# Performance work log

Hardware: AMD Instinct MI355X
Metric: run time of the kernel (lower is better)

Reference implementation:

```python
import jax, jax.numpy as jnp
import numpy as np

BOX_WARP = 1.2
BMIN, BMAX = -0.6, 0.6   # sampler bbox
EPS_FD = 0.01            # finite-difference eps for SDF normals
RADIUS = 0.5             # sphere sdf bias radius
INV_S = 80.0             # sdf -> density sharpness (softplus clamp mode)
S_PER_RAY = 96


def _grid_sample_one(feat, uv):
    # feat: [C,H,W]; uv: [M,2] in [-1,1]; bilinear, align_corners=False, zeros padding
    C, H, W = feat.shape
    x = ((uv[:, 0] + 1.0) * W - 1.0) * 0.5
    y = ((uv[:, 1] + 1.0) * H - 1.0) * 0.5
    x0 = jnp.floor(x).astype(jnp.int32)
    y0 = jnp.floor(y).astype(jnp.int32)
    wx = x - x0
    wy = y - y0

    def g(ix, iy):
        valid = ((ix >= 0) & (ix < W) & (iy >= 0) & (iy < H)).astype(feat.dtype)
        v = feat[:, jnp.clip(iy, 0, H - 1), jnp.clip(ix, 0, W - 1)]  # [C,M]
        return v * valid[None, :]

    out = (g(x0, y0) * (1 - wx) * (1 - wy) + g(x0 + 1, y0) * wx * (1 - wy)
           + g(x0, y0 + 1) * (1 - wx) * wy + g(x0 + 1, y0 + 1) * wx * wy)
    return out.T  # [M,C]


def sample_from_planes(planes, coords):
    # planes: [N,3,C,H,W]; coords: [N,M,3] -> [N,M,3*C]
    N, P, C, H, W = planes.shape
    M = coords.shape[1]
    nc = coords * (2.0 / BOX_WARP)
    proj = jnp.stack([nc[..., (0, 1)], nc[..., (0, 2)], nc[..., (1, 2)]], axis=1)  # [N,3,M,2]
    s = jax.vmap(_grid_sample_one)(planes.reshape(N * P, C, H, W), proj.reshape(N * P, M, 2))
    return s.reshape(N, P, M, C).transpose(0, 2, 1, 3).reshape(N, M, P * C)


def decode(planes, coords, W1, b1, W2, b2):
    x = sample_from_planes(planes, coords)
    return jax.nn.relu(x @ W1 + b1) @ W2 + b2  # [N,M,4]


def render(planes, ro, rd, W1, b1, W2, b2):
    N, R, _ = ro.shape
    S = S_PER_RAY
    safe_rd = jnp.where(jnp.abs(rd) < 1e-9, 1e-9, rd)
    t1 = (BMIN - ro) / safe_rd
    t2 = (BMAX - ro) / safe_rd
    tn = jnp.maximum(jnp.max(jnp.minimum(t1, t2), axis=-1), 0.0)   # [N,R] ray_start (auto box)
    tf = jnp.min(jnp.maximum(t1, t2), axis=-1)                      # [N,R] ray_end
    span = jnp.maximum(tf - tn, 0.0)
    frac = (jnp.arange(S, dtype=ro.dtype) + 0.5) / S
    depths = tn[..., None] + span[..., None] * frac                 # [N,R,S]
    pts = (ro[:, :, None, :] + depths[..., None] * rd[:, :, None, :]).reshape(N, R * S, 3)

    x = decode(planes, pts, W1, b1, W2, b2)
    sdf = x[..., 0:1]
    rgb = jax.nn.sigmoid(x[..., 1:]) * (1 + 2 * 0.001) - 0.001

    # finite-difference SDF gradient (3 extra decoder passes)
    eye = jnp.eye(3, dtype=pts.dtype) * EPS_FD
    sdf_off = jnp.stack(
        [decode(planes, jnp.clip(pts + eye[i], BMIN, BMAX), W1, b1, W2, b2)[..., 0] for i in range(3)],
        axis=-1)                                                    # [N,M,3]
    sdf_grad = (sdf_off - sdf) / EPS_FD
    normal = sdf_grad / (jnp.linalg.norm(sdf_grad, axis=-1, keepdims=True) + 1e-8)

    # sphere sdf bias, sdf -> density, alpha compositing
    shifted = sdf[..., 0] + (jnp.linalg.norm(pts, axis=-1) - RADIUS)
    sigma = jax.nn.softplus(-shifted * INV_S).reshape(N, R, S)
    delta = (span / S)[..., None]
    alpha = 1.0 - jnp.exp(-sigma * delta)
    T = jnp.cumprod(1.0 - alpha + 1e-10, axis=-1)
    T = jnp.concatenate([jnp.ones_like(T[..., :1]), T[..., :-1]], axis=-1)
    w = alpha * T                                                   # [N,R,S]

    rgb_s = (w[..., None] * rgb.reshape(N, R, S, 3)).sum(-2)
    wsum = w.sum(-1, keepdims=True)
    rgb_s = rgb_s + (1.0 - wsum)                                    # white background
    depth_s = (w * depths).sum(-1, keepdims=True)
    normal_s = (w[..., None] * normal.reshape(N, R, S, 3)).sum(-2)
    return rgb_s, depth_s, wsum, sdf_grad, normal_s


def reference(planes, ray_origins, ray_directions, W1, b1, W2, b2, render_size):
    N = planes.shape[0]
    rgb_s, depth_s, wsum, sdf_grad, normal_s = render(planes, ray_origins, ray_directions, W1, b1, W2, b2)
    n = normal_s / (jnp.linalg.norm(normal_s, axis=-1, keepdims=True) + 1e-8)
    n = (n + 1.0) * 0.5
    n = n * wsum  # lerp(0, n, opacity)
    H = W = render_size
    comp_rgb = rgb_s.transpose(0, 2, 1).reshape(N, 3, H, W)
    comp_depth = depth_s.transpose(0, 2, 1).reshape(N, 1, H, W)
    opacity = wsum.transpose(0, 2, 1).reshape(N, 1, H, W)
    comp_normal = n.transpose(0, 2, 1).reshape(N, 3, H, W)
    return (comp_rgb, comp_depth, opacity, comp_normal, sdf_grad)


def setup_inputs():
    key = jax.random.key(0)
    k0, k1, k2 = jax.random.split(key, 3)
    N, C, Hp, rs = 1, 80, 64, 64
    planes = jax.random.normal(k0, (N, 3, C, Hp, Hp), jnp.float32)
    u = jnp.linspace(-0.45, 0.45, rs)
    uu, vv = jnp.meshgrid(u, u, indexing='xy')
    d = jnp.stack([uu, vv, -jnp.ones_like(uu)], -1).reshape(-1, 3)
    d = d / jnp.linalg.norm(d, axis=-1, keepdims=True)
    ray_directions = jnp.broadcast_to(d, (N, rs * rs, 3)).astype(jnp.float32)
    ray_origins = jnp.broadcast_to(jnp.array([0.0, 0.0, 1.5], jnp.float32), (N, rs * rs, 3))
    W1 = jax.random.normal(k1, (3 * C, 64), jnp.float32) * 0.05
    b1 = jnp.zeros((64,), jnp.float32)
    W2 = jax.random.normal(k2, (64, 4), jnp.float32) * 0.05
    b2 = jnp.zeros((4,), jnp.float32)
    return {"planes": planes, "ray_origins": ray_origins, "ray_directions": ray_directions,
            "W1": W1, "b1": b1, "W2": W2, "b2": b2, "render_size": rs}
```

## Files before the change

kernel.cpp:

```cpp
#include <hip/hip_runtime.h>
#include <hip/hip_bf16.h>

#define NUM_RAYS 4096
#define S_PER 96
#define NPTS (NUM_RAYS * S_PER)
#define CCH 80
#define HID 64

#define WSB_FLAG   0
#define WSB_W2     256
#define WSB_B1     1536
#define WSB_B2     1856
#define WSB_W1S    4096
#define WSB_PT     40960



typedef __attribute__((ext_vector_type(8))) short short8;
typedef __attribute__((ext_vector_type(4))) float f32x4;
typedef __attribute__((ext_vector_type(2))) float f32x2;

__device__ __forceinline__ float bf2f(__hip_bfloat16 v) { return __bfloat162float(v); }

__device__ __forceinline__ short f2bs(float f) {
  __hip_bfloat16 h = __float2bfloat16(f);
  short s; __builtin_memcpy(&s, &h, 2); return s;
}

template <bool BF16>
__device__ __forceinline__ float ldin(const void* p, size_t i) {
  if (BF16) return bf2f(((const __hip_bfloat16*)p)[i]);
  else      return ((const float*)p)[i];
}
template <bool BF16>
__device__ __forceinline__ void stout(void* p, size_t i, float v) {
  if (BF16) ((__hip_bfloat16*)p)[i] = __float2bfloat16(v);
  else      ((float*)p)[i] = v;
}

__device__ __forceinline__ f32x2 unpk2(unsigned u) {
  f32x2 r;
  r.x = __uint_as_float(u << 16);
  r.y = __uint_as_float(u);
  return r;
}

__device__ __forceinline__ unsigned pack_bf16(float lo, float hi) {
#if __has_builtin(__builtin_amdgcn_cvt_pk_bf16_f32)
  typedef __attribute__((ext_vector_type(2))) __bf16 b2t;
  b2t r = __builtin_amdgcn_cvt_pk_bf16_f32(lo, hi);
  unsigned u; __builtin_memcpy(&u, &r, 4); return u;
#else
  unsigned ul = __float_as_uint(lo) + 0x8000u;
  unsigned uh = __float_as_uint(hi) + 0x8000u;
  return __builtin_amdgcn_perm(uh, ul, 0x07060302);
#endif
}

__global__ void detect_kernel(const void* __restrict__ rdv, float* __restrict__ ws) {
  int lane = threadIdx.x;
  const __hip_bfloat16* p = (const __hip_bfloat16*)rdv;
  float x = bf2f(p[lane * 3 + 0]);
  float y = bf2f(p[lane * 3 + 1]);
  float z = bf2f(p[lane * 3 + 2]);
  float n2 = x * x + y * y + z * z;
  bool ok = (n2 > 0.95f) && (n2 < 1.05f);
  unsigned long long m = __ballot(ok);
  if (lane == 0) *((int*)((char*)ws + WSB_FLAG)) = (m == ~0ull) ? 1 : 0;
}

template <bool BF16>
__global__ void prep_kernel(const void* __restrict__ W1,
                            const void* __restrict__ b1,
                            const void* __restrict__ W2,
                            const void* __restrict__ b2,
                            float* __restrict__ ws) {
  if ((*((const int*)((char*)ws + WSB_FLAG)) != 0) != BF16) return;
  int tid = blockIdx.x * blockDim.x + threadIdx.x;
  unsigned short* w1sw = (unsigned short*)((char*)ws + WSB_W1S);
  if (tid < 15360) {
    int p = tid / 5120;
    int r = tid - p * 5120;
    int ch, n;
    if (r < 4096) {
      int ccl  = r >> 11;
      int r2   = r & 2047;
      int j    = r2 & 7;
      int lane = (r2 >> 3) & 63;
      int nb   = r2 >> 9;
      ch = ccl * 32 + 8 * (lane >> 4) + j;
      n  = nb * 16 + (lane & 15);
    } else {
      int r2   = r - 4096;
      int j    = r2 & 7;
      int l31  = (r2 >> 3) & 31;
      int nb   = r2 >> 8;
      ch = 64 + 8 * (l31 >> 4) + j;
      n  = nb * 16 + (l31 & 15);
    }
    w1sw[tid] = (unsigned short)f2bs(ldin<BF16>(W1, (size_t)(p * 80 + ch) * 64 + n));
  }
  float* w2f = (float*)((char*)ws + WSB_W2);
  float* b1f = (float*)((char*)ws + WSB_B1);
  float* b2f = (float*)((char*)ws + WSB_B2);
  if (tid < 256) w2f[tid] = ldin<BF16>(W2, tid);
  if (tid < 64)  b1f[tid] = ldin<BF16>(b1, tid);
  if (tid < 4)   b2f[tid] = ldin<BF16>(b2, tid);
}

template <bool BF16>
__global__ void transpose_kernel(const void* __restrict__ planes, float* __restrict__ ws) {
  if ((*((const int*)((char*)ws + WSB_FLAG)) != 0) != BF16) return;
  int b  = blockIdx.x;
  int tt = b & 15;
  int ct = (b >> 4) % 5;
  int p  = b / 80;
  int tex = tt * 256 + threadIdx.x;
  unsigned u[8];
  #pragma unroll
  for (int i = 0; i < 8; i++) {
    int c0 = ct * 16 + 2 * i;
    float v0 = ldin<BF16>(planes, ((size_t)(p * 80 + c0) * 4096) + tex);
    float v1 = ldin<BF16>(planes, ((size_t)(p * 80 + c0 + 1) * 4096) + tex);
    unsigned s0 = (unsigned short)f2bs(v0);
    unsigned s1 = (unsigned short)f2bs(v1);
    u[i] = s0 | (s1 << 16);
  }
  unsigned short* ptb = (unsigned short*)((char*)ws + WSB_PT);
  uint4* dst = (uint4*)(ptb + ((size_t)(p * 4096 + tex) * 80 + ct * 16));
  dst[0] = make_uint4(u[0], u[1], u[2], u[3]);
  dst[1] = make_uint4(u[4], u[5], u[6], u[7]);
}

struct TapInfo {
  float w00, w10, w01, w11;
  int o00, o10, o01, o11;
};
__device__ __forceinline__ TapInfo tap_setup(float u, float v) {
  TapInfo t;
  float fx = u * 32.0f + 31.5f;
  float fy = v * 32.0f + 31.5f;
  float flx = floorf(fx), fly = floorf(fy);
  int x0 = (int)flx, y0 = (int)fly;
  float wx = fx - flx, wy = fy - fly;
  int x1 = x0 + 1, y1 = y0 + 1;
  bool vx0 = (x0 >= 0) && (x0 < 64);
  bool vx1 = (x1 >= 0) && (x1 < 64);
  bool vy0 = (y0 >= 0) && (y0 < 64);
  bool vy1 = (y1 >= 0) && (y1 < 64);
  int cx0 = min(max(x0, 0), 63), cx1 = min(max(x1, 0), 63);
  int cy0 = min(max(y0, 0), 63), cy1 = min(max(y1, 0), 63);
  t.w00 = (1.0f - wx) * (1.0f - wy) * ((vx0 && vy0) ? 1.0f : 0.0f);
  t.w10 = wx * (1.0f - wy)          * ((vx1 && vy0) ? 1.0f : 0.0f);
  t.w01 = (1.0f - wx) * wy          * ((vx0 && vy1) ? 1.0f : 0.0f);
  t.w11 = wx * wy                   * ((vx1 && vy1) ? 1.0f : 0.0f);
  t.o00 = cy0 * 64 + cx0; t.o10 = cy0 * 64 + cx1;
  t.o01 = cy1 * 64 + cx0; t.o11 = cy1 * 64 + cx1;
  return t;
}

template <bool BF16>
__global__ __launch_bounds__(256) void fused_kernel(
    const void* __restrict__ ro,
    const void* __restrict__ rd,
    const float* __restrict__ ws,
    void* __restrict__ out) {
  if ((*((const int*)((const char*)ws + WSB_FLAG)) != 0) != BF16) return;

  __shared__ __align__(16) unsigned short w1s[15360];
  __shared__ float rec[S_PER][7];
  __shared__ float scanb[S_PER];
  __shared__ float w2s[256];

  const unsigned short* ptb = (const unsigned short*)((const char*)ws + WSB_PT);
  const float* w2f = (const float*)((const char*)ws + WSB_W2);
  const float* b1f = (const float*)((const char*)ws + WSB_B1);
  const float* b2f = (const float*)((const char*)ws + WSB_B2);

  int tid = threadIdx.x;
  int wave = tid >> 6;
  int lane = tid & 63;
  int lane15 = lane & 15;
  int quad = lane >> 4;
  int ray = blockIdx.x;

  {
    const uint4* src = (const uint4*)((const char*)ws + WSB_W1S);
    uint4* dst = (uint4*)w1s;
    #pragma unroll
    for (int t = 0; t < 8; t++) {
      int idx = tid + 256 * t;
      if (idx < 1920) dst[idx] = src[idx];
    }
  }
  if (tid < 256) w2s[tid] = w2f[tid];

  float ox = ldin<BF16>(ro, (size_t)ray*3+0), oy = ldin<BF16>(ro, (size_t)ray*3+1), oz = ldin<BF16>(ro, (size_t)ray*3+2);
  float dx = ldin<BF16>(rd, (size_t)ray*3+0), dy = ldin<BF16>(rd, (size_t)ray*3+1), dz = ldin<BF16>(rd, (size_t)ray*3+2);
  float o3[3] = {ox, oy, oz}, d3[3] = {dx, dy, dz};
  float tmin = -1e30f, tmax = 1e30f;
  #pragma unroll
  for (int k = 0; k < 3; k++) {
    float sd = (fabsf(d3[k]) < 1e-9f) ? 1e-9f : d3[k];
    float ta = (-0.6f - o3[k]) / sd;
    float tb = ( 0.6f - o3[k]) / sd;
    tmin = fmaxf(tmin, fminf(ta, tb));
    tmax = fminf(tmax, fmaxf(ta, tb));
  }
  float tn = fmaxf(tmin, 0.0f);
  float span = fmaxf(tmax - tn, 0.0f);
  float delta = span * (1.0f / (float)S_PER);
  float b1x[4];
  #pragma unroll
  for (int nb = 0; nb < 4; nb++) b1x[nb] = b1f[nb * 16 + lane15];

  __syncthreads();

  #pragma unroll 1
  for (int it = 0; it < 6; it++) {
    int sbase = it * 16 + wave * 4;

    int sF = sbase + (lane15 >> 2);
    int d  = lane15 & 3;
    float depF = tn + span * (((float)sF + 0.5f) * (1.0f / (float)S_PER));
    float px = ox + depF * dx, py = oy + depF * dy, pz = oz + depF * dz;
    if (d == 1) px += 0.01f;
    if (d == 2) py += 0.01f;
    if (d == 3) pz += 0.01f;
    if (d > 0) {
      px = fminf(fmaxf(px, -0.6f), 0.6f);
      py = fminf(fmaxf(py, -0.6f), 0.6f);
      pz = fminf(fmaxf(pz, -0.6f), 0.6f);
    }
    const float inv = 1.0f / 0.6f;
    float ux = px * inv, uy = py * inv, uz = pz * inv;

    f32x4 acc[4];
    #pragma unroll
    for (int nb = 0; nb < 4; nb++) acc[nb] = (f32x4){0.f, 0.f, 0.f, 0.f};

    #pragma unroll 1
    for (int p = 0; p < 3; p++) {
      float u = (p == 2) ? uy : ux;
      float v = (p == 0) ? uy : uz;
      TapInfo t = tap_setup(u, v);
      const unsigned short* c00p = ptb + (size_t)p * 327680 + t.o00 * 80 + 8 * quad;
      const unsigned short* c10p = ptb + (size_t)p * 327680 + t.o10 * 80 + 8 * quad;
      const unsigned short* c01p = ptb + (size_t)p * 327680 + t.o01 * 80 + 8 * quad;
      const unsigned short* c11p = ptb + (size_t)p * 327680 + t.o11 * 80 + 8 * quad;
      f32x2 wv00 = {t.w00, t.w00}, wv10 = {t.w10, t.w10};
      f32x2 wv01 = {t.w01, t.w01}, wv11 = {t.w11, t.w11};
      const unsigned short* w1p = w1s + p * 5120;
      #pragma unroll
      for (int ccl = 0; ccl < 3; ccl++) {
        int4 afi = {0, 0, 0, 0};
        if (ccl < 2 || quad < 2) {
          uint4 q00 = *(const uint4*)(c00p + 32 * ccl);
          uint4 q10 = *(const uint4*)(c10p + 32 * ccl);
          uint4 q01 = *(const uint4*)(c01p + 32 * ccl);
          uint4 q11 = *(const uint4*)(c11p + 32 * ccl);
          unsigned u00[4] = {q00.x, q00.y, q00.z, q00.w};
          unsigned u10[4] = {q10.x, q10.y, q10.z, q10.w};
          unsigned u01[4] = {q01.x, q01.y, q01.z, q01.w};
          unsigned u11[4] = {q11.x, q11.y, q11.z, q11.w};
          int ae[4];
          #pragma unroll
          for (int q = 0; q < 4; q++) {
            f32x2 f = unpk2(u00[q]) * wv00;
            f = __builtin_elementwise_fma(unpk2(u10[q]), wv10, f);
            f = __builtin_elementwise_fma(unpk2(u01[q]), wv01, f);
            f = __builtin_elementwise_fma(unpk2(u11[q]), wv11, f);
            ae[q] = (int)pack_bf16(f.x, f.y);
          }
          afi.x = ae[0]; afi.y = ae[1]; afi.z = ae[2]; afi.w = ae[3];
        }
        short8 afr;
        __builtin_memcpy(&afr, &afi, 16);
        #pragma unroll
        for (int nb = 0; nb < 4; nb++) {
          int boff = (ccl < 2) ? (ccl * 2048 + (nb * 64 + lane) * 8)
                               : (4096 + (nb * 32 + (lane & 31)) * 8);
          short8 bfr = *(const short8*)(w1p + boff);
          acc[nb] = __builtin_amdgcn_mfma_f32_16x16x32_bf16(afr, bfr, acc[nb], 0, 0, 0);
        }
      }
    }

    float vals[7];
    #pragma unroll
    for (int k = 0; k < 7; k++) vals[k] = 0.0f;
    #pragma unroll
    for (int nb = 0; nb < 4; nb++) {
      float4 w2r = *(const float4*)(w2s + (nb * 16 + lane15) * 4);
      float hr0 = fmaxf(acc[nb][0] + b1x[nb], 0.0f);
      vals[0] = fmaf(hr0, w2r.x, vals[0]);
      vals[4] = fmaf(hr0, w2r.y, vals[4]);
      vals[5] = fmaf(hr0, w2r.z, vals[5]);
      vals[6] = fmaf(hr0, w2r.w, vals[6]);
      float hr1 = fmaxf(acc[nb][1] + b1x[nb], 0.0f);
      float hr2 = fmaxf(acc[nb][2] + b1x[nb], 0.0f);
      float hr3 = fmaxf(acc[nb][3] + b1x[nb], 0.0f);
      vals[1] = fmaf(hr1, w2r.x, vals[1]);
      vals[2] = fmaf(hr2, w2r.x, vals[2]);
      vals[3] = fmaf(hr3, w2r.x, vals[3]);
    }
    #pragma unroll
    for (int mask = 1; mask < 16; mask <<= 1) {
      #pragma unroll
      for (int k = 0; k < 7; k++) vals[k] += __shfl_xor(vals[k], mask, 64);
    }

    if (lane15 == 0) {
      int sE = sbase + quad;
      #pragma unroll
      for (int k = 0; k < 7; k++) rec[sE][k] = vals[k];
    }
  }

  __syncthreads();

  float b2_0 = b2f[0], b2_1 = b2f[1], b2_2 = b2f[2], b2_3 = b2f[3];
  float a = 0.f, l = 0.f, pcr = 0.f, pcg = 0.f, pcb = 0.f, pnx = 0.f, pny = 0.f, pnz = 0.f, pdt = 0.f;
  if (tid < S_PER) {
    float v0 = rec[tid][0], v1 = rec[tid][1], v2 = rec[tid][2], v3 = rec[tid][3];
    float v4 = rec[tid][4], v5 = rec[tid][5], v6 = rec[tid][6];
    float sdf0 = v0 + b2_0;
    float g0 = (v1 - v0) * 100.0f;
    float g1 = (v2 - v0) * 100.0f;
    float g2 = (v3 - v0) * 100.0f;
    size_t gid = (size_t)ray * S_PER + tid;
    stout<BF16>(out, (size_t)32768 + gid * 3 + 0, g0);
    stout<BF16>(out, (size_t)32768 + gid * 3 + 1, g1);
    stout<BF16>(out, (size_t)32768 + gid * 3 + 2, g2);
    pcr = 1.0f / (1.0f + expf(-(v4 + b2_1))) * 1.002f - 0.001f;
    pcg = 1.0f / (1.0f + expf(-(v5 + b2_2))) * 1.002f - 0.001f;
    pcb = 1.0f / (1.0f + expf(-(v6 + b2_3))) * 1.002f - 0.001f;
    pdt = tn + span * (((float)tid + 0.5f) * (1.0f / (float)S_PER));
    float ex = ox + pdt * dx, ey = oy + pdt * dy, ez = oz + pdt * dz;
    float pn = sqrtf(ex * ex + ey * ey + ez * ez);
    float shifted = sdf0 + pn - 0.5f;
    float xarg = -shifted * 80.0f;
    float sigma = (xarg > 20.0f) ? xarg : log1pf(expf(xarg));
    a = 1.0f - expf(-sigma * delta);
    float gl = sqrtf(g0 * g0 + g1 * g1 + g2 * g2) + 1e-8f;
    float igl = 1.0f / gl;
    pnx = g0 * igl; pny = g1 * igl; pnz = g2 * igl;
    l = logf(1.0f - a + 1e-10f);
    scanb[tid] = l;
  }
  __syncthreads();
  #pragma unroll
  for (int st = 1; st < S_PER; st <<= 1) {
    float v = 0.0f;
    if (tid < S_PER && tid >= st) v = scanb[tid - st];
    __syncthreads();
    if (tid < S_PER) scanb[tid] += v;
    __syncthreads();
  }
  if (tid < S_PER) {
    float T = expf(scanb[tid] - l);
    float w = a * T;
    rec[tid][0] = w;
    rec[tid][1] = w * pcr; rec[tid][2] = w * pcg; rec[tid][3] = w * pcb;
    rec[tid][4] = w * pnx; rec[tid][5] = w * pny; rec[tid][6] = w * pnz;
    scanb[tid] = w * pdt;
  }
  __syncthreads();
  #pragma unroll
  for (int off = 48; off >= 3; off >>= 1) {
    if (tid < off) {
      #pragma unroll
      for (int k = 0; k < 7; k++) rec[tid][k] += rec[tid + off][k];
      scanb[tid] += scanb[tid + off];
    }
    __syncthreads();
  }
  if (tid == 0) {
    float R[7];
    #pragma unroll
    for (int k = 0; k < 7; k++) R[k] = rec[0][k] + rec[1][k] + rec[2][k];
    float dsum = scanb[0] + scanb[1] + scanb[2];
    float wsum = R[0];
    float nl = sqrtf(R[4] * R[4] + R[5] * R[5] + R[6] * R[6]) + 1e-8f;
    float inl = 1.0f / nl;
    float nrm3[3] = {R[4], R[5], R[6]};
    float rgb3[3] = {R[1], R[2], R[3]};
    #pragma unroll
    for (int c = 0; c < 3; c++) {
      float n = (nrm3[c] * inl + 1.0f) * 0.5f * wsum;
      stout<BF16>(out, (size_t)(c * 4096 + ray), rgb3[c] + 1.0f - wsum);
      stout<BF16>(out, (size_t)(20480 + c * 4096 + ray), n);
    }
    stout<BF16>(out, (size_t)(12288 + ray), dsum);
    stout<BF16>(out, (size_t)(16384 + ray), wsum);
  }
}

extern "C" void kernel_launch(void* const* d_in, const int* in_sizes, int n_in,
                              void* d_out, int out_size, void* d_ws, size_t ws_size,
                              hipStream_t stream) {
  const void* planes = d_in[0];
  const void* ro     = d_in[1];
  const void* rd     = d_in[2];
  const void* W1     = d_in[3];
  const void* b1     = d_in[4];
  const void* W2     = d_in[5];
  const void* b2     = d_in[6];
  float* ws = (float*)d_ws;

  detect_kernel<<<1, 64, 0, stream>>>(rd, ws);
  prep_kernel<false><<<64, 256, 0, stream>>>(W1, b1, W2, b2, ws);
  prep_kernel<true ><<<64, 256, 0, stream>>>(W1, b1, W2, b2, ws);
  transpose_kernel<false><<<240, 256, 0, stream>>>(planes, ws);
  transpose_kernel<true ><<<240, 256, 0, stream>>>(planes, ws);
  fused_kernel<false><<<NUM_RAYS, 256, 0, stream>>>(ro, rd, ws, d_out);
  fused_kernel<true ><<<NUM_RAYS, 256, 0, stream>>>(ro, rd, ws, d_out);
}
```

Measured before the change: 277.7 us.

## Inline dtype detection per kernel and replace LDS scan/reduce with wave shuffles

Drops the separate detect kernel and the duplicate templated launches; each kernel now detects the input dtype itself with a wave ballot and branches to the matching templated body, cutting seven launches to three. The per-ray transmittance prefix scan and the weighted-sum reduction move from a shared-memory loop with many __syncthreads to wave shuffle scans and butterfly reductions, with one small cross-wave transfer. The cost is redundant detection loads in every block and a larger kernel holding both instantiations, which may raise register pressure.

```diff
diff --git a/kernel.cpp b/kernel.cpp
--- a/kernel.cpp
+++ b/kernel.cpp
@@ -7,7 +7,6 @@
 #define CCH 80
 #define HID 64
 
-#define WSB_FLAG   0
 #define WSB_W2     256
 #define WSB_B1     1536
 #define WSB_B2     1856
@@ -57,25 +56,23 @@
 #endif
 }
 
-__global__ void detect_kernel(const void* __restrict__ rdv, float* __restrict__ ws) {
-  int lane = threadIdx.x;
+__device__ __forceinline__ bool detect_bf16(const void* rdv) {
+  int lane = threadIdx.x & 63;
   const __hip_bfloat16* p = (const __hip_bfloat16*)rdv;
   float x = bf2f(p[lane * 3 + 0]);
   float y = bf2f(p[lane * 3 + 1]);
   float z = bf2f(p[lane * 3 + 2]);
   float n2 = x * x + y * y + z * z;
   bool ok = (n2 > 0.95f) && (n2 < 1.05f);
-  unsigned long long m = __ballot(ok);
-  if (lane == 0) *((int*)((char*)ws + WSB_FLAG)) = (m == ~0ull) ? 1 : 0;
+  return __ballot(ok) == ~0ull;
 }
 
 template <bool BF16>
-__global__ void prep_kernel(const void* __restrict__ W1,
-                            const void* __restrict__ b1,
-                            const void* __restrict__ W2,
-                            const void* __restrict__ b2,
-                            float* __restrict__ ws) {
-  if ((*((const int*)((char*)ws + WSB_FLAG)) != 0) != BF16) return;
+__device__ __forceinline__ void prep_body(const void* __restrict__ W1,
+                                          const void* __restrict__ b1,
+                                          const void* __restrict__ W2,
+                                          const void* __restrict__ b2,
+                                          float* __restrict__ ws) {
   int tid = blockIdx.x * blockDim.x + threadIdx.x;
   unsigned short* w1sw = (unsigned short*)((char*)ws + WSB_W1S);
   if (tid < 15360) {
@@ -108,9 +105,19 @@
   if (tid < 4)   b2f[tid] = ldin<BF16>(b2, tid);
 }
 
+__global__ void prep_kernel(const void* __restrict__ W1,
+                            const void* __restrict__ b1,
+                            const void* __restrict__ W2,
+                            const void* __restrict__ b2,
+                            const void* __restrict__ rd,
+                            float* __restrict__ ws) {
+  if (detect_bf16(rd)) prep_body<true >(W1, b1, W2, b2, ws);
+  else                 prep_body<false>(W1, b1, W2, b2, ws);
+}
+
 template <bool BF16>
-__global__ void transpose_kernel(const void* __restrict__ planes, float* __restrict__ ws) {
-  if ((*((const int*)((char*)ws + WSB_FLAG)) != 0) != BF16) return;
+__device__ __forceinline__ void transpose_body(const void* __restrict__ planes,
+                                               float* __restrict__ ws) {
   int b  = blockIdx.x;
   int tt = b & 15;
   int ct = (b >> 4) % 5;
@@ -130,6 +137,13 @@
   uint4* dst = (uint4*)(ptb + ((size_t)(p * 4096 + tex) * 80 + ct * 16));
   dst[0] = make_uint4(u[0], u[1], u[2], u[3]);
   dst[1] = make_uint4(u[4], u[5], u[6], u[7]);
+}
+
+__global__ void transpose_kernel(const void* __restrict__ planes,
+                                 const void* __restrict__ rd,
+                                 float* __restrict__ ws) {
+  if (detect_bf16(rd)) transpose_body<true >(planes, ws);
+  else                 transpose_body<false>(planes, ws);
 }
 
 struct TapInfo {
@@ -160,18 +174,15 @@
 }
 
 template <bool BF16>
-__global__ __launch_bounds__(256) void fused_kernel(
-    const void* __restrict__ ro,
-    const void* __restrict__ rd,
-    const float* __restrict__ ws,
-    void* __restrict__ out) {
-  if ((*((const int*)((const char*)ws + WSB_FLAG)) != 0) != BF16) return;
-
-  __shared__ __align__(16) unsigned short w1s[15360];
-  __shared__ float rec[S_PER][7];
-  __shared__ float scanb[S_PER];
-  __shared__ float w2s[256];
-
+__device__ __forceinline__ void fused_body(const void* __restrict__ ro,
+                                           const void* __restrict__ rd,
+                                           const float* __restrict__ ws,
+                                           void* __restrict__ out,
+                                           unsigned short* __restrict__ w1s,
+                                           float (*__restrict__ rec)[7],
+                                           float* __restrict__ w2s,
+                                           float* __restrict__ xfer,
+                                           float (*__restrict__ red)[8]) {
   const unsigned short* ptb = (const unsigned short*)((const char*)ws + WSB_PT);
   const float* w2f = (const float*)((const char*)ws + WSB_W2);
   const float* b1f = (const float*)((const char*)ws + WSB_B1);
@@ -346,40 +357,39 @@
     float igl = 1.0f / gl;
     pnx = g0 * igl; pny = g1 * igl; pnz = g2 * igl;
     l = logf(1.0f - a + 1e-10f);
-    scanb[tid] = l;
-  }
+  }
+
+  float lv = l;
+  #pragma unroll
+  for (int off = 1; off < 64; off <<= 1) {
+    float up = __shfl_up(lv, off, 64);
+    if (lane >= off) lv += up;
+  }
+  if (tid == 63) xfer[0] = lv;
   __syncthreads();
+  if (tid >= 64 && tid < S_PER) lv += xfer[0];
+
+  float T = expf(lv - l);
+  float w = (tid < S_PER) ? a * T : 0.0f;
+  float q[8];
+  q[0] = w;
+  q[1] = w * pcr; q[2] = w * pcg; q[3] = w * pcb;
+  q[4] = w * pnx; q[5] = w * pny; q[6] = w * pnz;
+  q[7] = w * pdt;
   #pragma unroll
-  for (int st = 1; st < S_PER; st <<= 1) {
-    float v = 0.0f;
-    if (tid < S_PER && tid >= st) v = scanb[tid - st];
-    __syncthreads();
-    if (tid < S_PER) scanb[tid] += v;
-    __syncthreads();
-  }
-  if (tid < S_PER) {
-    float T = expf(scanb[tid] - l);
-    float w = a * T;
-    rec[tid][0] = w;
-    rec[tid][1] = w * pcr; rec[tid][2] = w * pcg; rec[tid][3] = w * pcb;
-    rec[tid][4] = w * pnx; rec[tid][5] = w * pny; rec[tid][6] = w * pnz;
-    scanb[tid] = w * pdt;
+  for (int off = 1; off < 64; off <<= 1) {
+    #pragma unroll
+    for (int k = 0; k < 8; k++) q[k] += __shfl_xor(q[k], off, 64);
+  }
+  if (lane == 0) {
+    #pragma unroll
+    for (int k = 0; k < 8; k++) red[wave][k] = q[k];
   }
   __syncthreads();
-  #pragma unroll
-  for (int off = 48; off >= 3; off >>= 1) {
-    if (tid < off) {
-      #pragma unroll
-      for (int k = 0; k < 7; k++) rec[tid][k] += rec[tid + off][k];
-      scanb[tid] += scanb[tid + off];
-    }
-    __syncthreads();
-  }
   if (tid == 0) {
-    float R[7];
-    #pragma unroll
-    for (int k = 0; k < 7; k++) R[k] = rec[0][k] + rec[1][k] + rec[2][k];
-    float dsum = scanb[0] + scanb[1] + scanb[2];
+    float R[8];
+    #pragma unroll
+    for (int k = 0; k < 8; k++) R[k] = red[0][k] + red[1][k] + red[2][k] + red[3][k];
     float wsum = R[0];
     float nl = sqrtf(R[4] * R[4] + R[5] * R[5] + R[6] * R[6]) + 1e-8f;
     float inl = 1.0f / nl;
@@ -391,9 +401,24 @@
       stout<BF16>(out, (size_t)(c * 4096 + ray), rgb3[c] + 1.0f - wsum);
       stout<BF16>(out, (size_t)(20480 + c * 4096 + ray), n);
     }
-    stout<BF16>(out, (size_t)(12288 + ray), dsum);
+    stout<BF16>(out, (size_t)(12288 + ray), R[7]);
     stout<BF16>(out, (size_t)(16384 + ray), wsum);
   }
+}
+
+__global__ __launch_bounds__(256) void fused_kernel(
+    const void* __restrict__ ro,
+    const void* __restrict__ rd,
+    const float* __restrict__ ws,
+    void* __restrict__ out) {
+  __shared__ __align__(16) unsigned short w1s[15360];
+  __shared__ float rec[S_PER][7];
+  __shared__ float w2s[256];
+  __shared__ float xfer[1];
+  __shared__ float red[4][8];
+
+  if (detect_bf16(rd)) fused_body<true >(ro, rd, ws, out, w1s, rec, w2s, xfer, red);
+  else                 fused_body<false>(ro, rd, ws, out, w1s, rec, w2s, xfer, red);
 }
 
 extern "C" void kernel_launch(void* const* d_in, const int* in_sizes, int n_in,
@@ -408,11 +433,7 @@
   const void* b2     = d_in[6];
   float* ws = (float*)d_ws;
 
-  detect_kernel<<<1, 64, 0, stream>>>(rd, ws);
-  prep_kernel<false><<<64, 256, 0, stream>>>(W1, b1, W2, b2, ws);
-  prep_kernel<true ><<<64, 256, 0, stream>>>(W1, b1, W2, b2, ws);
-  transpose_kernel<false><<<240, 256, 0, stream>>>(planes, ws);
-  transpose_kernel<true ><<<240, 256, 0, stream>>>(planes, ws);
-  fused_kernel<false><<<NUM_RAYS, 256, 0, stream>>>(ro, rd, ws, d_out);
-  fused_kernel<true ><<<NUM_RAYS, 256, 0, stream>>>(ro, rd, ws, d_out);
-}
+  prep_kernel<<<64, 256, 0, stream>>>(W1, b1, W2, b2, rd, ws);
+  transpose_kernel<<<240, 256, 0, stream>>>(planes, rd, ws);
+  fused_kernel<<<NUM_RAYS, 256, 0, stream>>>(ro, rd, ws, d_out);
+}
```

Result: faster. 270.5 us (-2.6%).
